# Optimization experiments

Hardware: AMD Instinct MI355X
Metric: run time of the kernel (lower is better)

The kernel has to match this reference:

```python
import jax, jax.numpy as jnp
import numpy as np

B, S, H = 4, 1024, 1024
N_HEADS = 16
HEAD_DIM = H // N_HEADS


def setup_inputs() -> dict:
    key = jax.random.key(0)
    ks = jax.random.split(key, 7)
    scale = 1.0 / np.sqrt(H)
    return {
        "hidden_states": jax.random.normal(ks[0], (B, S, H), dtype=jnp.float32),
        "Wq": jax.random.normal(ks[1], (H, H), dtype=jnp.float32) * scale,
        "bq": jnp.zeros((H,), dtype=jnp.float32),
        "Wk": jax.random.normal(ks[2], (H, H), dtype=jnp.float32) * scale,
        "bk": jnp.zeros((H,), dtype=jnp.float32),
        "Wv": jax.random.normal(ks[3], (H, H), dtype=jnp.float32) * scale,
        "bv": jnp.zeros((H,), dtype=jnp.float32),
    }


def _split_heads(x):
    # [B,S,H] -> [B,h,S,d]
    Bx, Sx, _ = x.shape
    return x.reshape(Bx, Sx, N_HEADS, HEAD_DIM).transpose(0, 2, 1, 3)


def reference(hidden_states, Wq, bq, Wk, bk, Wv, bv):
    q = _split_heads(hidden_states @ Wq + bq)  # [B,h,S,d]
    k = _split_heads(hidden_states @ Wk + bk)
    v = _split_heads(hidden_states @ Wv + bv)
    scores = jnp.einsum("bhqd,bhkd->bhqk", q, k) / jnp.sqrt(
        jnp.asarray(HEAD_DIM, dtype=q.dtype)
    )
    probs = jax.nn.softmax(scores, axis=-1)  # dropout is identity in eval
    ctx = jnp.einsum("bhqk,bhkd->bhqd", probs, v)  # [B,h,S,d]
    return ctx.transpose(0, 2, 1, 3).reshape(B, S, H)
```

## Files before the change

kernel.cpp:

```cpp
#include <hip/hip_runtime.h>
#include <hip/hip_bf16.h>

typedef __bf16 bf16_t;
typedef float f32x4 __attribute__((ext_vector_type(4)));
typedef __bf16 bf16x8 __attribute__((ext_vector_type(8)));


__device__ __forceinline__ void g2lds16(const void* g, void* l) {
  __builtin_amdgcn_global_load_lds(
      (const __attribute__((address_space(1))) void*)g,
      (__attribute__((address_space(3))) void*)l, 16, 0, 0);
}

__global__ __launch_bounds__(256) void convert_x(const float* __restrict__ X,
                                                 bf16_t* __restrict__ Xb) {
  int i = (blockIdx.x * 256 + threadIdx.x) * 8;
  float4 a = *(const float4*)(X + i);
  float4 b = *(const float4*)(X + i + 4);
  bf16x8 o;
  o[0] = (bf16_t)a.x; o[1] = (bf16_t)a.y; o[2] = (bf16_t)a.z; o[3] = (bf16_t)a.w;
  o[4] = (bf16_t)b.x; o[5] = (bf16_t)b.y; o[6] = (bf16_t)b.z; o[7] = (bf16_t)b.w;
  *(bf16x8*)(Xb + i) = o;
}

__global__ __launch_bounds__(256) void transpose_w(const float* __restrict__ Wq,
                                                   const float* __restrict__ Wk,
                                                   const float* __restrict__ Wv,
                                                   bf16_t* __restrict__ Wtb) {
  __shared__ float tile[32][33];
  const float* W = blockIdx.y == 0 ? Wq : (blockIdx.y == 1 ? Wk : Wv);
  const int k0 = (blockIdx.x >> 5) * 32, n0 = (blockIdx.x & 31) * 32;
  const int tx = threadIdx.x & 31, ty = threadIdx.x >> 5;
#pragma unroll
  for (int i = 0; i < 32; i += 8)
    tile[ty + i][tx] = W[(size_t)(k0 + ty + i) * 1024 + n0 + tx];
  __syncthreads();
#pragma unroll
  for (int i = 0; i < 32; i += 8)
    Wtb[(size_t)(blockIdx.y * 1024 + n0 + ty + i) * 1024 + k0 + tx] =
        (bf16_t)tile[tx][ty + i];
}

__global__ __launch_bounds__(256) void gemm_qkv(const bf16_t* __restrict__ Xb,
                                                const bf16_t* __restrict__ Wtb,
                                                const float* __restrict__ bq,
                                                const float* __restrict__ bk,
                                                const float* __restrict__ bv,
                                                bf16_t* __restrict__ Cc) {
  __shared__ __align__(16) bf16_t As[128 * 32];
  __shared__ __align__(16) bf16_t Bs[128 * 32];
  const int t = threadIdx.x, lane = t & 63, wave = t >> 6;
  const int g = lane >> 4, r16 = lane & 15;
  const int wg = (blockIdx.x & 7) * 96 + (blockIdx.x >> 3);
  const int tm = wg / 24, tn = wg % 24;
  const int m0 = tm * 128, n0 = tn * 128;
  const int wr = wave >> 1, wc = wave & 1;
  f32x4 zero4 = {0.f, 0.f, 0.f, 0.f};
  f32x4 acc[4][4];
#pragma unroll
  for (int i = 0; i < 4; ++i)
#pragma unroll
    for (int j = 0; j < 4; ++j) acc[i][j] = zero4;
  const int sr = t >> 2, sk = (t & 3) * 8;
  for (int k0 = 0; k0 < 1024; k0 += 32) {
    g2lds16(&Xb[(size_t)(m0 + sr) * 1024 + k0 + sk], (char*)As + wave * 1024);
    g2lds16(&Xb[(size_t)(m0 + 64 + sr) * 1024 + k0 + sk], (char*)As + 4096 + wave * 1024);
    g2lds16(&Wtb[(size_t)(n0 + sr) * 1024 + k0 + sk], (char*)Bs + wave * 1024);
    g2lds16(&Wtb[(size_t)(n0 + 64 + sr) * 1024 + k0 + sk], (char*)Bs + 4096 + wave * 1024);
    __syncthreads();
    bf16x8 af[4], bfr[4];
#pragma unroll
    for (int i = 0; i < 4; ++i)
      af[i] = *(const bf16x8*)&As[(wr * 64 + i * 16 + r16) * 32 + g * 8];
#pragma unroll
    for (int j = 0; j < 4; ++j)
      bfr[j] = *(const bf16x8*)&Bs[(wc * 64 + j * 16 + r16) * 32 + g * 8];
#pragma unroll
    for (int i = 0; i < 4; ++i)
#pragma unroll
      for (int j = 0; j < 4; ++j)
        acc[i][j] = __builtin_amdgcn_mfma_f32_16x16x32_bf16(af[i], bfr[j], acc[i][j], 0, 0, 0);
    __syncthreads();
  }
#pragma unroll
  for (int j = 0; j < 4; ++j) {
    int col = n0 + wc * 64 + j * 16 + r16;
    float bias = col < 1024 ? bq[col] : (col < 2048 ? bk[col - 1024] : bv[col - 2048]);
#pragma unroll
    for (int i = 0; i < 4; ++i)
#pragma unroll
      for (int r = 0; r < 4; ++r) {
        int row = m0 + wr * 64 + i * 16 + g * 4 + r;
        Cc[(size_t)row * 3072 + col] = (bf16_t)(acc[i][j][r] + bias);
      }
  }
}

__global__ __launch_bounds__(256) void vtrans(const bf16_t* __restrict__ Cc,
                                              bf16_t* __restrict__ Vt) {
  __shared__ bf16_t tile[32][34];
  const int bh = blockIdx.x >> 6, tloc = blockIdx.x & 63;
  const int s0 = (tloc >> 1) * 32, d0 = (tloc & 1) * 32;
  const int b = bh >> 4, h = bh & 15;
  const int tx = threadIdx.x & 31, ty = threadIdx.x >> 5;
#pragma unroll
  for (int i = 0; i < 32; i += 8)
    tile[ty + i][tx] =
        Cc[(size_t)(b * 1024 + s0 + ty + i) * 3072 + 2048 + h * 64 + d0 + tx];
  __syncthreads();
#pragma unroll
  for (int i = 0; i < 32; i += 8)
    Vt[((size_t)bh * 64 + d0 + ty + i) * 1024 + s0 + tx] = tile[tx][ty + i];
}

__global__ __launch_bounds__(512) void attn_fwd(const bf16_t* __restrict__ Cc,
                                                const bf16_t* __restrict__ Vt,
                                                float* __restrict__ out) {
  __shared__ __align__(16) bf16_t Ks[2][64 * 64];
  __shared__ __align__(16) bf16_t Vts[2][64 * 64];
  __shared__ __align__(16) bf16_t P_lds[8][16][72];
  const int t = threadIdx.x, lane = t & 63, wave = t >> 6;
  const int g = lane >> 4, r16 = lane & 15;
  const int lb = (blockIdx.x & 7) * 64 + (blockIdx.x >> 3);
  const int qb = lb & 7;
  const int bh = lb >> 3;
  const int b = bh >> 4, h = bh & 15;
  const size_t crow0 = (size_t)b * 1024;

  const int qrow = qb * 128 + wave * 16 + r16;
  bf16x8 qf0 = *(const bf16x8*)&Cc[(crow0 + qrow) * 3072 + h * 64 + g * 8];
  bf16x8 qf1 = *(const bf16x8*)&Cc[(crow0 + qrow) * 3072 + h * 64 + 32 + g * 8];

  f32x4 zero4 = {0.f, 0.f, 0.f, 0.f};
  f32x4 ctx[4];
#pragma unroll
  for (int dt = 0; dt < 4; ++dt) ctx[dt] = zero4;
  f32x4 l_lane = zero4;
  const float C2 = 0.125f * 1.44269504f;

  const int kr = t >> 3;
  const int swc = ((t & 7) ^ (kr & 7)) * 8;
  const int ksl0 = (g ^ (r16 & 7)) * 8;
  const int ksl1 = ksl0 ^ 32;
  const bf16_t* Vth = Vt + (size_t)bh * 65536;

  auto stage = [&](int buf, int kt2) {
    const int ks0 = kt2 * 64;
    g2lds16(&Cc[(crow0 + ks0 + kr) * 3072 + 1024 + h * 64 + swc],
            (char*)&Ks[buf][0] + wave * 1024);
    g2lds16(&Vth[(size_t)kr * 1024 + ks0 + swc],
            (char*)&Vts[buf][0] + wave * 1024);
  };

  stage(0, 0);
  __syncthreads();
  int cur = 0;

  for (int kt = 0; kt < 16; ++kt) {
    if (kt < 15) stage(cur ^ 1, kt + 1);

    f32x4 s[4];
#pragma unroll
    for (int jt = 0; jt < 4; ++jt) {
      const bf16_t* kro = &Ks[cur][(jt * 16 + r16) * 64];
      bf16x8 kb0 = *(const bf16x8*)(kro + ksl0);
      bf16x8 kb1 = *(const bf16x8*)(kro + ksl1);
      f32x4 z = __builtin_amdgcn_mfma_f32_16x16x32_bf16(qf0, kb0, zero4, 0, 0, 0);
      s[jt] = __builtin_amdgcn_mfma_f32_16x16x32_bf16(qf1, kb1, z, 0, 0, 0);
    }

#pragma unroll
    for (int jt = 0; jt < 4; ++jt)
#pragma unroll
      for (int r = 0; r < 4; ++r) {
        float pv = exp2f(s[jt][r] * C2);
        l_lane[r] += pv;
        P_lds[wave][g * 4 + r][jt * 16 + r16] = (bf16_t)pv;
      }

    bf16x8 pa0 = *(const bf16x8*)&P_lds[wave][r16][g * 8];
    bf16x8 pa1 = *(const bf16x8*)&P_lds[wave][r16][32 + g * 8];
#pragma unroll
    for (int dt = 0; dt < 4; ++dt) {
      const bf16_t* vro = &Vts[cur][(dt * 16 + r16) * 64];
      bf16x8 vb0 = *(const bf16x8*)(vro + ksl0);
      bf16x8 vb1 = *(const bf16x8*)(vro + ksl1);
      ctx[dt] = __builtin_amdgcn_mfma_f32_16x16x32_bf16(pa0, vb0, ctx[dt], 0, 0, 0);
      ctx[dt] = __builtin_amdgcn_mfma_f32_16x16x32_bf16(pa1, vb1, ctx[dt], 0, 0, 0);
    }
    __syncthreads();
    cur ^= 1;
  }

#pragma unroll
  for (int m = 1; m < 16; m <<= 1)
#pragma unroll
    for (int r = 0; r < 4; ++r) l_lane[r] += __shfl_xor(l_lane[r], m, 64);

#pragma unroll
  for (int dt = 0; dt < 4; ++dt)
#pragma unroll
    for (int r = 0; r < 4; ++r) {
      int row = qb * 128 + wave * 16 + g * 4 + r;
      out[(crow0 + row) * 1024 + h * 64 + dt * 16 + r16] = ctx[dt][r] / l_lane[r];
    }
}

extern "C" void kernel_launch(void* const* d_in, const int* in_sizes, int n_in,
                              void* d_out, int out_size, void* d_ws, size_t ws_size,
                              hipStream_t stream) {
  const float* X  = (const float*)d_in[0];
  const float* Wq = (const float*)d_in[1];
  const float* bq = (const float*)d_in[2];
  const float* Wk = (const float*)d_in[3];
  const float* bk = (const float*)d_in[4];
  const float* Wv = (const float*)d_in[5];
  const float* bv = (const float*)d_in[6];
  float* out = (float*)d_out;
  char* ws = (char*)d_ws;
  bf16_t* Xb  = (bf16_t*)(ws);
  bf16_t* Wtb = (bf16_t*)(ws + 8388608);
  bf16_t* Cc  = (bf16_t*)(ws + 14680064);
  bf16_t* Vt  = (bf16_t*)(ws + 39845888);

  convert_x<<<2048, 256, 0, stream>>>(X, Xb);
  transpose_w<<<dim3(1024, 3), 256, 0, stream>>>(Wq, Wk, Wv, Wtb);
  gemm_qkv<<<768, 256, 0, stream>>>(Xb, Wtb, bq, bk, bv, Cc);
  vtrans<<<4096, 256, 0, stream>>>(Cc, Vt);
  attn_fwd<<<512, 512, 0, stream>>>(Cc, Vt, out);
}
```

Measured before the change: 173.1 us.

## Fuse prep kernels, write V transposed from GEMM epilogue, vectorize stores

Merges the X conversion and weight transpose into one launch, and drops the separate V-transpose kernel by having the QKV GEMM write V directly in transposed layout. For the Q/K tiles it swaps the MFMA operand order so each lane holds four consecutive columns, which allows 8-byte bf16x4 stores. The attention epilogue likewise swaps operands so each lane writes a float4, and it redistributes the row sums with a shuffle. This removes two launches and one round trip of V through memory, but adds branches inside the GEMM and relies on getting the transposed fragment indexing right.

Result: no change. 170.1 us (-1.8%).

```diff
diff --git a/kernel.cpp b/kernel.cpp
--- a/kernel.cpp
+++ b/kernel.cpp
@@ -3,6 +3,7 @@
 
 typedef __bf16 bf16_t;
 typedef float f32x4 __attribute__((ext_vector_type(4)));
+typedef __bf16 bf16x4 __attribute__((ext_vector_type(4)));
 typedef __bf16 bf16x8 __attribute__((ext_vector_type(8)));
 
 
@@ -12,33 +13,36 @@
       (__attribute__((address_space(3))) void*)l, 16, 0, 0);
 }
 
-__global__ __launch_bounds__(256) void convert_x(const float* __restrict__ X,
-                                                 bf16_t* __restrict__ Xb) {
-  int i = (blockIdx.x * 256 + threadIdx.x) * 8;
-  float4 a = *(const float4*)(X + i);
-  float4 b = *(const float4*)(X + i + 4);
-  bf16x8 o;
-  o[0] = (bf16_t)a.x; o[1] = (bf16_t)a.y; o[2] = (bf16_t)a.z; o[3] = (bf16_t)a.w;
-  o[4] = (bf16_t)b.x; o[5] = (bf16_t)b.y; o[6] = (bf16_t)b.z; o[7] = (bf16_t)b.w;
-  *(bf16x8*)(Xb + i) = o;
-}
-
-__global__ __launch_bounds__(256) void transpose_w(const float* __restrict__ Wq,
-                                                   const float* __restrict__ Wk,
-                                                   const float* __restrict__ Wv,
-                                                   bf16_t* __restrict__ Wtb) {
+__global__ __launch_bounds__(256) void prep(const float* __restrict__ X,
+                                            const float* __restrict__ Wq,
+                                            const float* __restrict__ Wk,
+                                            const float* __restrict__ Wv,
+                                            bf16_t* __restrict__ Xb,
+                                            bf16_t* __restrict__ Wtb) {
   __shared__ float tile[32][33];
-  const float* W = blockIdx.y == 0 ? Wq : (blockIdx.y == 1 ? Wk : Wv);
-  const int k0 = (blockIdx.x >> 5) * 32, n0 = (blockIdx.x & 31) * 32;
-  const int tx = threadIdx.x & 31, ty = threadIdx.x >> 5;
-#pragma unroll
-  for (int i = 0; i < 32; i += 8)
-    tile[ty + i][tx] = W[(size_t)(k0 + ty + i) * 1024 + n0 + tx];
-  __syncthreads();
-#pragma unroll
-  for (int i = 0; i < 32; i += 8)
-    Wtb[(size_t)(blockIdx.y * 1024 + n0 + ty + i) * 1024 + k0 + tx] =
-        (bf16_t)tile[tx][ty + i];
+  if (blockIdx.x < 2048) {
+    int i = (blockIdx.x * 256 + threadIdx.x) * 8;
+    float4 a = *(const float4*)(X + i);
+    float4 b = *(const float4*)(X + i + 4);
+    bf16x8 o;
+    o[0] = (bf16_t)a.x; o[1] = (bf16_t)a.y; o[2] = (bf16_t)a.z; o[3] = (bf16_t)a.w;
+    o[4] = (bf16_t)b.x; o[5] = (bf16_t)b.y; o[6] = (bf16_t)b.z; o[7] = (bf16_t)b.w;
+    *(bf16x8*)(Xb + i) = o;
+  } else {
+    const int bid = blockIdx.x - 2048;
+    const int wsel = bid >> 10, bx = bid & 1023;
+    const float* W = wsel == 0 ? Wq : (wsel == 1 ? Wk : Wv);
+    const int k0 = (bx >> 5) * 32, n0 = (bx & 31) * 32;
+    const int tx = threadIdx.x & 31, ty = threadIdx.x >> 5;
+#pragma unroll
+    for (int i = 0; i < 32; i += 8)
+      tile[ty + i][tx] = W[(size_t)(k0 + ty + i) * 1024 + n0 + tx];
+    __syncthreads();
+#pragma unroll
+    for (int i = 0; i < 32; i += 8)
+      Wtb[(size_t)(wsel * 1024 + n0 + ty + i) * 1024 + k0 + tx] =
+          (bf16_t)tile[tx][ty + i];
+  }
 }
 
 __global__ __launch_bounds__(256) void gemm_qkv(const bf16_t* __restrict__ Xb,
@@ -46,7 +50,8 @@
                                                 const float* __restrict__ bq,
                                                 const float* __restrict__ bk,
                                                 const float* __restrict__ bv,
-                                                bf16_t* __restrict__ Cc) {
+                                                bf16_t* __restrict__ Cc,
+                                                bf16_t* __restrict__ Vt) {
   __shared__ __align__(16) bf16_t As[128 * 32];
   __shared__ __align__(16) bf16_t Bs[128 * 32];
   const int t = threadIdx.x, lane = t & 63, wave = t >> 6;
@@ -54,6 +59,7 @@
   const int wg = (blockIdx.x & 7) * 96 + (blockIdx.x >> 3);
   const int tm = wg / 24, tn = wg % 24;
   const int m0 = tm * 128, n0 = tn * 128;
+  const bool isV = (n0 >= 2048);
   const int wr = wave >> 1, wc = wave & 1;
   f32x4 zero4 = {0.f, 0.f, 0.f, 0.f};
   f32x4 acc[4][4];
@@ -75,42 +81,61 @@
 #pragma unroll
     for (int j = 0; j < 4; ++j)
       bfr[j] = *(const bf16x8*)&Bs[(wc * 64 + j * 16 + r16) * 32 + g * 8];
-#pragma unroll
-    for (int i = 0; i < 4; ++i)
-#pragma unroll
-      for (int j = 0; j < 4; ++j)
-        acc[i][j] = __builtin_amdgcn_mfma_f32_16x16x32_bf16(af[i], bfr[j], acc[i][j], 0, 0, 0);
-    __syncthreads();
-  }
-#pragma unroll
-  for (int j = 0; j < 4; ++j) {
-    int col = n0 + wc * 64 + j * 16 + r16;
-    float bias = col < 1024 ? bq[col] : (col < 2048 ? bk[col - 1024] : bv[col - 2048]);
-#pragma unroll
-    for (int i = 0; i < 4; ++i)
-#pragma unroll
-      for (int r = 0; r < 4; ++r) {
-        int row = m0 + wr * 64 + i * 16 + g * 4 + r;
-        Cc[(size_t)row * 3072 + col] = (bf16_t)(acc[i][j][r] + bias);
+    if (!isV) {
+#pragma unroll
+      for (int i = 0; i < 4; ++i)
+#pragma unroll
+        for (int j = 0; j < 4; ++j)
+          acc[i][j] = __builtin_amdgcn_mfma_f32_16x16x32_bf16(bfr[j], af[i], acc[i][j], 0, 0, 0);
+    } else {
+#pragma unroll
+      for (int i = 0; i < 4; ++i)
+#pragma unroll
+        for (int j = 0; j < 4; ++j)
+          acc[i][j] = __builtin_amdgcn_mfma_f32_16x16x32_bf16(af[i], bfr[j], acc[i][j], 0, 0, 0);
+    }
+    __syncthreads();
+  }
+  if (!isV) {
+    const float* barr = (n0 < 1024) ? bq : bk;
+    const int bbase = n0 - ((n0 < 1024) ? 0 : 1024) + wc * 64;
+    float4 bias4[4];
+#pragma unroll
+    for (int j = 0; j < 4; ++j)
+      bias4[j] = *(const float4*)&barr[bbase + j * 16 + g * 4];
+#pragma unroll
+    for (int j = 0; j < 4; ++j) {
+      const int col0 = n0 + wc * 64 + j * 16 + g * 4;
+#pragma unroll
+      for (int i = 0; i < 4; ++i) {
+        const int row = m0 + wr * 64 + i * 16 + r16;
+        bf16x4 o;
+        o[0] = (bf16_t)(acc[i][j][0] + bias4[j].x);
+        o[1] = (bf16_t)(acc[i][j][1] + bias4[j].y);
+        o[2] = (bf16_t)(acc[i][j][2] + bias4[j].z);
+        o[3] = (bf16_t)(acc[i][j][3] + bias4[j].w);
+        *(bf16x4*)&Cc[(size_t)row * 3072 + col0] = o;
       }
-  }
-}
-
-__global__ __launch_bounds__(256) void vtrans(const bf16_t* __restrict__ Cc,
-                                              bf16_t* __restrict__ Vt) {
-  __shared__ bf16_t tile[32][34];
-  const int bh = blockIdx.x >> 6, tloc = blockIdx.x & 63;
-  const int s0 = (tloc >> 1) * 32, d0 = (tloc & 1) * 32;
-  const int b = bh >> 4, h = bh & 15;
-  const int tx = threadIdx.x & 31, ty = threadIdx.x >> 5;
-#pragma unroll
-  for (int i = 0; i < 32; i += 8)
-    tile[ty + i][tx] =
-        Cc[(size_t)(b * 1024 + s0 + ty + i) * 3072 + 2048 + h * 64 + d0 + tx];
-  __syncthreads();
-#pragma unroll
-  for (int i = 0; i < 32; i += 8)
-    Vt[((size_t)bh * 64 + d0 + ty + i) * 1024 + s0 + tx] = tile[tx][ty + i];
+    }
+  } else {
+#pragma unroll
+    for (int j = 0; j < 4; ++j) {
+      const int dglob = n0 - 2048 + wc * 64 + j * 16 + r16;
+      const float bvj = bv[dglob];
+      const int h = dglob >> 6, d = dglob & 63;
+#pragma unroll
+      for (int i = 0; i < 4; ++i) {
+        const int row = m0 + wr * 64 + i * 16 + g * 4;
+        const int b = row >> 10, s = row & 1023;
+        bf16x4 o;
+        o[0] = (bf16_t)(acc[i][j][0] + bvj);
+        o[1] = (bf16_t)(acc[i][j][1] + bvj);
+        o[2] = (bf16_t)(acc[i][j][2] + bvj);
+        o[3] = (bf16_t)(acc[i][j][3] + bvj);
+        *(bf16x4*)&Vt[((size_t)(b * 16 + h) * 64 + d) * 1024 + s] = o;
+      }
+    }
+  }
 }
 
 __global__ __launch_bounds__(512) void attn_fwd(const bf16_t* __restrict__ Cc,
@@ -185,8 +210,8 @@
       const bf16_t* vro = &Vts[cur][(dt * 16 + r16) * 64];
       bf16x8 vb0 = *(const bf16x8*)(vro + ksl0);
       bf16x8 vb1 = *(const bf16x8*)(vro + ksl1);
-      ctx[dt] = __builtin_amdgcn_mfma_f32_16x16x32_bf16(pa0, vb0, ctx[dt], 0, 0, 0);
-      ctx[dt] = __builtin_amdgcn_mfma_f32_16x16x32_bf16(pa1, vb1, ctx[dt], 0, 0, 0);
+      ctx[dt] = __builtin_amdgcn_mfma_f32_16x16x32_bf16(vb0, pa0, ctx[dt], 0, 0, 0);
+      ctx[dt] = __builtin_amdgcn_mfma_f32_16x16x32_bf16(vb1, pa1, ctx[dt], 0, 0, 0);
     }
     __syncthreads();
     cur ^= 1;
@@ -196,14 +221,20 @@
   for (int m = 1; m < 16; m <<= 1)
 #pragma unroll
     for (int r = 0; r < 4; ++r) l_lane[r] += __shfl_xor(l_lane[r], m, 64);
-
-#pragma unroll
-  for (int dt = 0; dt < 4; ++dt)
-#pragma unroll
-    for (int r = 0; r < 4; ++r) {
-      int row = qb * 128 + wave * 16 + g * 4 + r;
-      out[(crow0 + row) * 1024 + h * 64 + dt * 16 + r16] = ctx[dt][r] / l_lane[r];
-    }
+  float lr[4];
+#pragma unroll
+  for (int r = 0; r < 4; ++r) lr[r] = __shfl(l_lane[r], (r16 >> 2) << 4, 64);
+  const int rs = r16 & 3;
+  const float lden = rs == 0 ? lr[0] : (rs == 1 ? lr[1] : (rs == 2 ? lr[2] : lr[3]));
+  const float rinv = 1.0f / lden;
+
+  const int q = qb * 128 + wave * 16 + r16;
+#pragma unroll
+  for (int dt = 0; dt < 4; ++dt) {
+    float4 o = {ctx[dt][0] * rinv, ctx[dt][1] * rinv, ctx[dt][2] * rinv,
+                ctx[dt][3] * rinv};
+    *(float4*)&out[(crow0 + q) * 1024 + h * 64 + dt * 16 + g * 4] = o;
+  }
 }
 
 extern "C" void kernel_launch(void* const* d_in, const int* in_sizes, int n_in,
@@ -223,9 +254,7 @@
   bf16_t* Cc  = (bf16_t*)(ws + 14680064);
   bf16_t* Vt  = (bf16_t*)(ws + 39845888);
 
-  convert_x<<<2048, 256, 0, stream>>>(X, Xb);
-  transpose_w<<<dim3(1024, 3), 256, 0, stream>>>(Wq, Wk, Wv, Wtb);
-  gemm_qkv<<<768, 256, 0, stream>>>(Xb, Wtb, bq, bk, bv, Cc);
-  vtrans<<<4096, 256, 0, stream>>>(Cc, Vt);
+  prep<<<5120, 256, 0, stream>>>(X, Wq, Wk, Wv, Xb, Wtb);
+  gemm_qkv<<<768, 256, 0, stream>>>(Xb, Wtb, bq, bk, bv, Cc, Vt);
   attn_fwd<<<512, 512, 0, stream>>>(Cc, Vt, out);
 }
```
